# Kernel tuning notes

Measured on AMD Instinct MI355X. Metric: run time of the kernel, lower is better.

Reference implementation:

```python
import jax, jax.numpy as jnp
import numpy as np

D_MODEL = 64
D_K = 64
N_HEADS = 4
D_FF = 64
LN_EPS = 1e-5


def _layernorm(x, g, b):
    mu = jnp.mean(x, axis=-1, keepdims=True)
    var = jnp.var(x, axis=-1, keepdims=True)
    return (x - mu) * jax.lax.rsqrt(var + LN_EPS) * g + b


def setup_inputs() -> dict:
    key = jax.random.key(0)
    ks = jax.random.split(key, 20)
    B, L = 8, 2048
    s = 0.05
    inp = {
        "x": jax.random.normal(ks[0], (B, L, D_MODEL), jnp.float32),
        "attn_mask": jax.random.randint(ks[1], (B, L, L), 0, 2).astype(bool),
        "u": jax.random.normal(ks[2], (B, 1, D_MODEL), jnp.float32),
        "wq": jax.random.normal(ks[3], (D_MODEL, D_K * N_HEADS), jnp.float32) * s,
        "wk": jax.random.normal(ks[4], (D_MODEL, D_K * N_HEADS), jnp.float32) * s,
        "wv": jax.random.normal(ks[5], (D_MODEL, D_K * N_HEADS), jnp.float32) * s,
        "uqw": jax.random.normal(ks[6], (D_MODEL, D_K), jnp.float32) * s,
        "ukw": jax.random.normal(ks[7], (D_MODEL, D_K), jnp.float32) * s,
        "uvw": jax.random.normal(ks[8], (D_MODEL, D_K), jnp.float32) * s,
        "sq1": jax.random.normal(ks[9], (D_MODEL, D_MODEL // 2), jnp.float32) * s,
        "sq2": jax.random.normal(ks[10], (D_MODEL // 2, 1), jnp.float32) * s,
        "sk1": jax.random.normal(ks[11], (D_MODEL, D_MODEL // 2), jnp.float32) * s,
        "sk2": jax.random.normal(ks[12], (D_MODEL // 2, 1), jnp.float32) * s,
        "sv1": jax.random.normal(ks[13], (D_MODEL, D_MODEL // 2), jnp.float32) * s,
        "sv2": jax.random.normal(ks[14], (D_MODEL // 2, 1), jnp.float32) * s,
        "fcw": jax.random.normal(ks[15], (N_HEADS * D_K, D_MODEL), jnp.float32) * s,
        "ln1_g": jnp.ones((D_MODEL,), jnp.float32),
        "ln1_b": jnp.zeros((D_MODEL,), jnp.float32),
        "ffn1": jax.random.normal(ks[16], (D_MODEL, D_FF), jnp.float32) * s,
        "ffn2": jax.random.normal(ks[17], (D_FF, D_MODEL), jnp.float32) * s,
        "ln2_g": jnp.ones((D_MODEL,), jnp.float32),
        "ln2_b": jnp.zeros((D_MODEL,), jnp.float32),
    }
    return inp


def reference(x, attn_mask, u, wq, wk, wv, uqw, ukw, uvw, sq1, sq2, sk1, sk2,
              sv1, sv2, fcw, ln1_g, ln1_b, ffn1, ffn2, ln2_g, ln2_b):
    B, L, _ = x.shape
    H, dk = N_HEADS, D_K
    # per-head Q,K,V: [B,H,L,dk]
    Q = (x @ wq).reshape(B, L, H, dk).transpose(0, 2, 1, 3)
    K = (x @ wk).reshape(B, L, H, dk).transpose(0, 2, 1, 3)
    V = (x @ wv).reshape(B, L, H, dk).transpose(0, 2, 1, 3)
    # broadcast scalar gates from u: [B,1,1]
    S_q = jax.nn.relu(u @ sq1) @ sq2
    S_k = jax.nn.relu(u @ sk1) @ sk2
    S_v = jax.nn.relu(u @ sv1) @ sv2
    uQ = (x @ uqw) * S_q  # [B,L,dk]
    uK = (x @ ukw) * S_k
    uV = (x @ uvw) * S_v
    scores = (jnp.einsum('bhqd,bhkd->bhqk', Q, K)
              + jnp.einsum('bqd,bkd->bqk', uQ, uK)[:, None]) / jnp.sqrt(
                  jnp.asarray(dk, x.dtype))
    scores = jnp.where(attn_mask[:, None], jnp.asarray(-1e9, x.dtype), scores)
    attn = jax.nn.softmax(scores, axis=-1)  # [B,H,L,L]
    ctx = jnp.einsum('bhqk,bhkd->bhqd', attn, V + uV[:, None])
    ctx = ctx.transpose(0, 2, 1, 3).reshape(B, L, H * dk)
    out = ctx @ fcw  # dropout is identity in eval mode
    enc = _layernorm(out + x, ln1_g, ln1_b)
    ffn = jax.nn.relu(enc @ ffn1) @ ffn2
    res = _layernorm(ffn + enc, ln2_g, ln2_b)
    return (res, attn)
```

## Files before the change

kernel.cpp:

```cpp
#include <hip/hip_runtime.h>
#include <hip/hip_bf16.h>
#include <stdint.h>

typedef __bf16  bf16x8  __attribute__((ext_vector_type(8)));
typedef float   f32x4   __attribute__((ext_vector_type(4)));
typedef unsigned short u16x8 __attribute__((ext_vector_type(8)));
typedef unsigned short u16x4 __attribute__((ext_vector_type(4)));
typedef unsigned short ushort_t;

__device__ __forceinline__ unsigned short f2b(float f) {
    __hip_bfloat16 h = __float2bfloat16(f);
    return *reinterpret_cast<unsigned short*>(&h);
}

__device__ __forceinline__ void cp16(const void* g, void* l) {
    __builtin_amdgcn_global_load_lds(
        (const __attribute__((address_space(1))) unsigned int*)g,
        (__attribute__((address_space(3))) unsigned int*)l,
        16, 0, 0);
}

#define BB 8
#define LL 2048
#define DM 64
#define NH 4
#define DK 64

__global__ __launch_bounds__(256) void k_maskpack(const int* __restrict__ mask,
                                                  unsigned int* __restrict__ words) {
    int tid = blockIdx.x * 256 + threadIdx.x;
    const int4* p = reinterpret_cast<const int4*>(mask) + (size_t)tid * 8;
    unsigned int wbits = 0u;
    #pragma unroll
    for (int i = 0; i < 8; i++) {
        int4 v = p[i];
        wbits |= (v.x != 0 ? 1u << (4 * i + 0) : 0u);
        wbits |= (v.y != 0 ? 1u << (4 * i + 1) : 0u);
        wbits |= (v.z != 0 ? 1u << (4 * i + 2) : 0u);
        wbits |= (v.w != 0 ? 1u << (4 * i + 3) : 0u);
    }
    words[tid] = wbits;
}

__global__ __launch_bounds__(64) void k_gates(const float* __restrict__ u,
                                              const float* s1q, const float* s2q,
                                              const float* s1k, const float* s2k,
                                              const float* s1v, const float* s2v,
                                              float* __restrict__ gates) {
    int b = blockIdx.x, g = blockIdx.y, lane = threadIdx.x;
    const float* s1 = (g == 0) ? s1q : (g == 1) ? s1k : s1v;
    const float* s2 = (g == 0) ? s2q : (g == 1) ? s2k : s2v;
    float ur = u[b * 64 + lane];
    float acc = 0.f;
    for (int j = 0; j < 64; j++) {
        float uj = __shfl(ur, j, 64);
        if (lane < 32) acc += uj * s1[j * 32 + lane];
    }
    float r = (lane < 32) ? fmaxf(acc, 0.f) * s2[lane] : 0.f;
    for (int m = 32; m >= 1; m >>= 1) r += __shfl_xor(r, m, 64);
    if (lane == 0) gates[b * 3 + g] = r;
}

__global__ __launch_bounds__(256) void k_proj(const float* __restrict__ x,
                                              const float* __restrict__ wq,
                                              const float* __restrict__ wk,
                                              const float* __restrict__ wv,
                                              const float* __restrict__ uqw,
                                              const float* __restrict__ ukw,
                                              const float* __restrict__ uvw,
                                              const float* __restrict__ gates,
                                              ushort_t* __restrict__ Qe,
                                              ushort_t* __restrict__ Ke,
                                              ushort_t* __restrict__ VeT) {
    int lt = blockIdx.x, b = blockIdx.y, t = threadIdx.x;
    int l0 = lt * 32;
    __shared__ float lx[32][68];
    __shared__ float luv[32][68];
    #pragma unroll
    for (int i = 0; i < 2; i++) {
        int id = t + i * 256;
        int r = id >> 4, c4 = id & 15;
        float4 v = *(const float4*)&x[((b * LL) + l0 + r) * 64 + c4 * 4];
        *(float4*)&lx[r][c4 * 4] = v;
    }
    __syncthreads();
    float Sq = gates[b * 3 + 0], Sk = gates[b * 3 + 1], Sv = gates[b * 3 + 2];
    if (t < 192) {
        int m = t >> 6, d = t & 63;
        const float* uw = (m == 0) ? uqw : (m == 1) ? ukw : uvw;
        float acc[32];
        #pragma unroll
        for (int r = 0; r < 32; r++) acc[r] = 0.f;
        for (int j = 0; j < 64; j += 4) {
            float w0 = uw[(j + 0) * 64 + d], w1 = uw[(j + 1) * 64 + d];
            float w2 = uw[(j + 2) * 64 + d], w3 = uw[(j + 3) * 64 + d];
            #pragma unroll
            for (int r = 0; r < 32; r++) {
                float4 xv = *(const float4*)&lx[r][j];
                acc[r] += xv.x * w0 + xv.y * w1 + xv.z * w2 + xv.w * w3;
            }
        }
        if (m == 2) {
            #pragma unroll
            for (int r = 0; r < 32; r++) luv[r][d] = acc[r] * Sv;
        } else if (m == 0) {
            for (int r = 0; r < 32; r++) {
                unsigned short v = f2b(acc[r] * Sq * 0.125f);
                int base = ((b * NH) * LL + l0 + r) * 128 + 64 + d;
                #pragma unroll
                for (int hh2 = 0; hh2 < 4; hh2++) Qe[base + hh2 * (LL * 128)] = v;
            }
        } else {
            for (int r = 0; r < 32; r++) {
                unsigned short v = f2b(acc[r] * Sk);
                int col = 64 + (d ^ ((r & 7) << 3));
                int base = ((b * NH) * LL + l0 + r) * 128 + col;
                #pragma unroll
                for (int hh2 = 0; hh2 < 4; hh2++) Ke[base + hh2 * (LL * 128)] = v;
            }
        }
    }
    __syncthreads();
    int c = t, hh = c >> 6, d = c & 63;
    float aq_[32], ak_[32], av_[32];
    #pragma unroll
    for (int r = 0; r < 32; r++) { aq_[r] = 0.f; ak_[r] = 0.f; av_[r] = 0.f; }
    for (int j = 0; j < 64; j += 4) {
        float q0w = wq[(j + 0) * 256 + c], q1w = wq[(j + 1) * 256 + c];
        float q2w = wq[(j + 2) * 256 + c], q3w = wq[(j + 3) * 256 + c];
        float k0w = wk[(j + 0) * 256 + c], k1w = wk[(j + 1) * 256 + c];
        float k2w = wk[(j + 2) * 256 + c], k3w = wk[(j + 3) * 256 + c];
        float v0w = wv[(j + 0) * 256 + c], v1w = wv[(j + 1) * 256 + c];
        float v2w = wv[(j + 2) * 256 + c], v3w = wv[(j + 3) * 256 + c];
        #pragma unroll
        for (int r = 0; r < 32; r++) {
            float4 xv = *(const float4*)&lx[r][j];
            aq_[r] += xv.x * q0w + xv.y * q1w + xv.z * q2w + xv.w * q3w;
            ak_[r] += xv.x * k0w + xv.y * k1w + xv.z * k2w + xv.w * k3w;
            av_[r] += xv.x * v0w + xv.y * v1w + xv.z * v2w + xv.w * v3w;
        }
    }
    int outbase = (b * NH + hh) * LL + l0;
    #pragma unroll
    for (int r = 0; r < 32; r++) Qe[(outbase + r) * 128 + d] = f2b(aq_[r] * 0.125f);
    #pragma unroll
    for (int r = 0; r < 32; r++)
        Ke[(outbase + r) * 128 + (d ^ ((r & 7) << 3))] = f2b(ak_[r]);
    long vbase = ((long)(b * NH + hh) * 64 + d) * LL;
    int lblk = l0 & ~63, loff = l0 & 63;
    #pragma unroll
    for (int rb = 0; rb < 4; rb++) {
        u16x8 vv;
        #pragma unroll
        for (int k = 0; k < 8; k++) {
            int r = rb * 8 + k;
            vv[k] = f2b(av_[r] + luv[r][d]);
        }
        int off = (loff + rb * 8) ^ ((d & 7) << 3);
        *(u16x8*)&VeT[vbase + lblk + off] = vv;
    }
}

__global__ __launch_bounds__(256) void k_attn(const ushort_t* __restrict__ Qe,
                                              const ushort_t* __restrict__ Ke,
                                              const ushort_t* __restrict__ VeT,
                                              const unsigned int* __restrict__ mwords,
                                              float* __restrict__ ctx,
                                              float* __restrict__ attn) {
    int lin = blockIdx.x + 32 * blockIdx.y + 128 * blockIdx.z;
    int sw  = ((lin & 7) << 7) | (lin >> 3);
    int qt = sw & 31, h = (sw >> 5) & 3, b = sw >> 7;

    int t = threadIdx.x, w = t >> 6, lane = t & 63, quad = lane >> 4, l15 = lane & 15;
    int q0 = qt * 64;
    int bh = b * NH + h;
    const ushort_t* QeB = Qe + (long)bh * LL * 128;
    const ushort_t* KeB = Ke + (long)bh * LL * 128;
    const ushort_t* VtB = VeT + (long)bh * 64 * LL;
    float* attnB = attn + (long)bh * LL * LL;
    const unsigned int* mB = mwords + (long)(b * LL) * 64;

    __shared__ ushort_t sKe[2][64 * 128];
    __shared__ ushort_t sVT[2][64 * 64];
    __shared__ unsigned int smask[64][66];
    __shared__ ushort_t sPb[4][16][72];

    #pragma unroll
    for (int i = 0; i < 16; i++) {
        int id = t + i * 256;
        smask[id >> 6][id & 63] = mB[(q0 + (id >> 6)) * 64 + (id & 63)];
    }

    bf16x8 aq[4];
    int qrow = q0 + w * 16 + l15;
    #pragma unroll
    for (int c = 0; c < 4; c++)
        aq[c] = *(const bf16x8*)&QeB[qrow * 128 + c * 32 + quad * 8];

    int swz = (l15 & 7) << 3;
    float lsum = 0.f;

    #pragma unroll
    for (int i = 0; i < 4; i++) {
        int off = (t + i * 256) * 16;
        cp16((const char*)KeB + off, (char*)&sKe[0][0] + off);
    }
    for (int kt = 0; kt < 32; kt++) {
        int cur = kt & 1;
        __syncthreads();
        if (kt < 31) {
            size_t gb = (size_t)(kt + 1) * 64 * 256;
            #pragma unroll
            for (int i = 0; i < 4; i++) {
                int off = (t + i * 256) * 16;
                cp16((const char*)KeB + gb + off, (char*)&sKe[cur ^ 1][0] + off);
            }
        }
        #pragma unroll
        for (int nb = 0; nb < 4; nb++) {
            f32x4 s = (f32x4){0.f, 0.f, 0.f, 0.f};
            #pragma unroll
            for (int c = 0; c < 4; c++) {
                bf16x8 kb = *(const bf16x8*)&sKe[cur][(nb * 16 + l15) * 128 + ((c * 32 + quad * 8) ^ swz)];
                s = __builtin_amdgcn_mfma_f32_16x16x32_bf16(kb, aq[c], s, 0, 0, 0);
            }
            unsigned int word = smask[w * 16 + l15][kt * 2 + (nb >> 1)];
            #pragma unroll
            for (int reg = 0; reg < 4; reg++) {
                unsigned int bit = (word >> ((nb & 1) * 16 + quad * 4 + reg)) & 1u;
                lsum += bit ? 0.f : __expf(fminf(s[reg], 60.f));
            }
        }
    }
    {
        lsum += __shfl_xor(lsum, 16, 64);
        lsum += __shfl_xor(lsum, 32, 64);
    }
    float inv = (lsum > 0.f) ? 1.f / lsum : 0.f;
    float invC[4];
    #pragma unroll
    for (int reg = 0; reg < 4; reg++) invC[reg] = __shfl(inv, quad * 4 + reg, 16);

    f32x4 cacc[4];
    #pragma unroll
    for (int db = 0; db < 4; db++) cacc[db] = (f32x4){0.f, 0.f, 0.f, 0.f};

    #pragma unroll
    for (int i = 0; i < 4; i++) {
        int off = (t + i * 256) * 16;
        cp16((const char*)KeB + off, (char*)&sKe[0][0] + off);
    }
    #pragma unroll
    for (int i = 0; i < 2; i++) {
        int off = (t + i * 256) * 16;
        int d = off >> 7, cb = off & 127;
        cp16((const char*)VtB + (size_t)d * (LL * 2) + cb, (char*)&sVT[0][0] + off);
    }
    for (int kt = 0; kt < 32; kt++) {
        int cur = kt & 1;
        int k0 = kt * 64;
        __syncthreads();
        if (kt < 31) {
            size_t gKe = (size_t)(k0 + 64) * 256;
            #pragma unroll
            for (int i = 0; i < 4; i++) {
                int off = (t + i * 256) * 16;
                cp16((const char*)KeB + gKe + off, (char*)&sKe[cur ^ 1][0] + off);
            }
            #pragma unroll
            for (int i = 0; i < 2; i++) {
                int off = (t + i * 256) * 16;
                int d = off >> 7, cb = off & 127;
                cp16((const char*)VtB + (size_t)d * (LL * 2) + (size_t)(k0 + 64) * 2 + cb,
                     (char*)&sVT[cur ^ 1][0] + off);
            }
        }
        #pragma unroll
        for (int nb = 0; nb < 4; nb++) {
            f32x4 s = (f32x4){0.f, 0.f, 0.f, 0.f};
            #pragma unroll
            for (int c = 0; c < 4; c++) {
                bf16x8 kb = *(const bf16x8*)&sKe[cur][(nb * 16 + l15) * 128 + ((c * 32 + quad * 8) ^ swz)];
                s = __builtin_amdgcn_mfma_f32_16x16x32_bf16(kb, aq[c], s, 0, 0, 0);
            }
            unsigned int word = smask[w * 16 + l15][kt * 2 + (nb >> 1)];
            u16x4 pk;
            f32x4 st;
            #pragma unroll
            for (int reg = 0; reg < 4; reg++) {
                unsigned int bit = (word >> ((nb & 1) * 16 + quad * 4 + reg)) & 1u;
                float p = bit ? 0.f : __expf(fminf(s[reg], 60.f));
                pk[reg] = f2b(p);
                st[reg] = p * inv;
            }
            *(u16x4*)&sPb[w][l15][nb * 16 + quad * 4] = pk;
            __builtin_nontemporal_store(st,
                (f32x4*)&attnB[(long)(q0 + w * 16 + l15) * LL + k0 + nb * 16 + quad * 4]);
        }
        #pragma unroll
        for (int db = 0; db < 4; db++) {
            #pragma unroll
            for (int c2 = 0; c2 < 2; c2++) {
                bf16x8 a  = *(const bf16x8*)&sPb[w][l15][c2 * 32 + quad * 8];
                bf16x8 bb = *(const bf16x8*)&sVT[cur][(db * 16 + l15) * 64 + ((c2 * 32 + quad * 8) ^ swz)];
                cacc[db] = __builtin_amdgcn_mfma_f32_16x16x32_bf16(a, bb, cacc[db], 0, 0, 0);
            }
        }
    }
    #pragma unroll
    for (int db = 0; db < 4; db++)
        #pragma unroll
        for (int reg = 0; reg < 4; reg++) {
            int qr = q0 + w * 16 + quad * 4 + reg;
            ctx[((long)(b * LL) + qr) * 256 + h * 64 + db * 16 + l15] = cacc[db][reg] * invC[reg];
        }
}

__global__ __launch_bounds__(256) void k_epi(const float* __restrict__ ctx,
                                             const float* __restrict__ x,
                                             const float* __restrict__ fcw,
                                             const float* __restrict__ g1,
                                             const float* __restrict__ b1,
                                             const float* __restrict__ f1,
                                             const float* __restrict__ f2,
                                             const float* __restrict__ g2,
                                             const float* __restrict__ b2w,
                                             float* __restrict__ res) {
    int w = threadIdx.x >> 6, lane = threadIdx.x & 63;
    int row = blockIdx.x * 4 + w;
    const float* cr = ctx + (long)row * 256;
    float creg[4];
    #pragma unroll
    for (int i = 0; i < 4; i++) creg[i] = cr[i * 64 + lane];
    float acc = 0.f;
    #pragma unroll
    for (int j = 0; j < 256; j++) {
        float cj = __shfl(creg[j >> 6], j & 63, 64);
        acc += cj * fcw[j * 64 + lane];
    }
    float val = acc + x[row * 64 + lane];
    float mu = val;
    #pragma unroll
    for (int m = 1; m < 64; m <<= 1) mu += __shfl_xor(mu, m, 64);
    mu *= (1.f / 64.f);
    float d0 = val - mu;
    float var = d0 * d0;
    #pragma unroll
    for (int m = 1; m < 64; m <<= 1) var += __shfl_xor(var, m, 64);
    var *= (1.f / 64.f);
    float enc = d0 * rsqrtf(var + 1e-5f) * g1[lane] + b1[lane];
    float a1 = 0.f;
    #pragma unroll
    for (int j = 0; j < 64; j++) a1 += __shfl(enc, j, 64) * f1[j * 64 + lane];
    float hrel = fmaxf(a1, 0.f);
    float a2 = 0.f;
    #pragma unroll
    for (int j = 0; j < 64; j++) a2 += __shfl(hrel, j, 64) * f2[j * 64 + lane];
    float v2 = a2 + enc;
    float mu2 = v2;
    #pragma unroll
    for (int m = 1; m < 64; m <<= 1) mu2 += __shfl_xor(mu2, m, 64);
    mu2 *= (1.f / 64.f);
    float d2 = v2 - mu2;
    float var2 = d2 * d2;
    #pragma unroll
    for (int m = 1; m < 64; m <<= 1) var2 += __shfl_xor(var2, m, 64);
    var2 *= (1.f / 64.f);
    float outv = d2 * rsqrtf(var2 + 1e-5f) * g2[lane] + b2w[lane];
    res[row * 64 + lane] = outv;
}

extern "C" void kernel_launch(void* const* d_in, const int* in_sizes, int n_in,
                              void* d_out, int out_size, void* d_ws, size_t ws_size,
                              hipStream_t stream) {
    const float* x    = (const float*)d_in[0];
    const int*   mask = (const int*)d_in[1];
    const float* u    = (const float*)d_in[2];
    const float* wq   = (const float*)d_in[3];
    const float* wk   = (const float*)d_in[4];
    const float* wv   = (const float*)d_in[5];
    const float* uqw  = (const float*)d_in[6];
    const float* ukw  = (const float*)d_in[7];
    const float* uvw  = (const float*)d_in[8];
    const float* sq1  = (const float*)d_in[9];
    const float* sq2  = (const float*)d_in[10];
    const float* sk1  = (const float*)d_in[11];
    const float* sk2  = (const float*)d_in[12];
    const float* sv1  = (const float*)d_in[13];
    const float* sv2  = (const float*)d_in[14];
    const float* fcw  = (const float*)d_in[15];
    const float* g1   = (const float*)d_in[16];
    const float* b1   = (const float*)d_in[17];
    const float* f1   = (const float*)d_in[18];
    const float* f2   = (const float*)d_in[19];
    const float* g2   = (const float*)d_in[20];
    const float* b2w  = (const float*)d_in[21];

    char* ws = (char*)d_ws;
    float*        gates  = (float*)(ws + 0);
    unsigned int* mwords = (unsigned int*)(ws + 4096);
    ushort_t*     Qe     = (ushort_t*)(ws + 4198400);
    ushort_t*     Ke     = (ushort_t*)(ws + 20975616);
    ushort_t*     VeT    = (ushort_t*)(ws + 37752832);
    float*        ctx    = (float*)(ws + 46141440);

    float* res  = (float*)d_out;
    float* attn = (float*)d_out + (size_t)BB * LL * DM;

    k_maskpack<<<dim3(4096), dim3(256), 0, stream>>>(mask, mwords);
    k_gates<<<dim3(8, 3), dim3(64), 0, stream>>>(u, sq1, sq2, sk1, sk2, sv1, sv2, gates);
    k_proj<<<dim3(64, 8), dim3(256), 0, stream>>>(x, wq, wk, wv, uqw, ukw, uvw, gates, Qe, Ke, VeT);
    k_attn<<<dim3(32, 4, 8), dim3(256), 0, stream>>>(Qe, Ke, VeT, mwords, ctx, attn);
    k_epi<<<dim3(4096), dim3(256), 0, stream>>>(ctx, x, fcw, g1, b1, f1, f2, g2, b2w, res);
}
```

Measured before the change: 1.019 ms.

## Stream mask words via async LDS loads and coalesce attn stores through shared

Replaces the upfront load of the whole 64x64 mask-word tile into shared memory with a double-buffered async load of 4 words per row, issued every other key tile. The attention-probability stores are staged through a per-wave shared buffer so each global nontemporal store writes contiguous 128-byte row segments instead of scattered 16-byte pieces. This aims to improve coalescing of the dominant attn write stream and cut mask-loading overhead and LDS footprint. The cost is extra LDS traffic and possible bank conflicts on the staging buffer.

```diff
diff --git a/kernel.cpp b/kernel.cpp
--- a/kernel.cpp
+++ b/kernel.cpp
@@ -182,14 +182,9 @@
 
     __shared__ ushort_t sKe[2][64 * 128];
     __shared__ ushort_t sVT[2][64 * 64];
-    __shared__ unsigned int smask[64][66];
     __shared__ ushort_t sPb[4][16][72];
-
-    #pragma unroll
-    for (int i = 0; i < 16; i++) {
-        int id = t + i * 256;
-        smask[id >> 6][id & 63] = mB[(q0 + (id >> 6)) * 64 + (id & 63)];
-    }
+    __shared__ float    sSt[4][16][68];
+    __shared__ unsigned int msk[2][64][4];
 
     bf16x8 aq[4];
     int qrow = q0 + w * 16 + l15;
@@ -199,12 +194,15 @@
 
     int swz = (l15 & 7) << 3;
     float lsum = 0.f;
+    int srow = lane >> 3, scol = lane & 7;
 
     #pragma unroll
     for (int i = 0; i < 4; i++) {
         int off = (t + i * 256) * 16;
         cp16((const char*)KeB + off, (char*)&sKe[0][0] + off);
     }
+    if (w == 0)
+        cp16((const char*)&mB[(q0 + lane) * 64], (char*)&msk[0][0][0] + lane * 16);
     for (int kt = 0; kt < 32; kt++) {
         int cur = kt & 1;
         __syncthreads();
@@ -216,6 +214,10 @@
                 cp16((const char*)KeB + gb + off, (char*)&sKe[cur ^ 1][0] + off);
             }
         }
+        if ((kt & 1) == 0 && kt < 30 && w == 0)
+            cp16((const char*)&mB[(q0 + lane) * 64 + kt * 2 + 4],
+                 (char*)&msk[((kt >> 1) & 1) ^ 1][0][0] + lane * 16);
+        uint2 mw = *(const uint2*)&msk[(kt >> 1) & 1][w * 16 + l15][(kt & 1) * 2];
         #pragma unroll
         for (int nb = 0; nb < 4; nb++) {
             f32x4 s = (f32x4){0.f, 0.f, 0.f, 0.f};
@@ -224,7 +226,7 @@
                 bf16x8 kb = *(const bf16x8*)&sKe[cur][(nb * 16 + l15) * 128 + ((c * 32 + quad * 8) ^ swz)];
                 s = __builtin_amdgcn_mfma_f32_16x16x32_bf16(kb, aq[c], s, 0, 0, 0);
             }
-            unsigned int word = smask[w * 16 + l15][kt * 2 + (nb >> 1)];
+            unsigned int word = (nb & 2) ? mw.y : mw.x;
             #pragma unroll
             for (int reg = 0; reg < 4; reg++) {
                 unsigned int bit = (word >> ((nb & 1) * 16 + quad * 4 + reg)) & 1u;
@@ -256,6 +258,8 @@
         int d = off >> 7, cb = off & 127;
         cp16((const char*)VtB + (size_t)d * (LL * 2) + cb, (char*)&sVT[0][0] + off);
     }
+    if (w == 0)
+        cp16((const char*)&mB[(q0 + lane) * 64], (char*)&msk[0][0][0] + lane * 16);
     for (int kt = 0; kt < 32; kt++) {
         int cur = kt & 1;
         int k0 = kt * 64;
@@ -275,6 +279,10 @@
                      (char*)&sVT[cur ^ 1][0] + off);
             }
         }
+        if ((kt & 1) == 0 && kt < 30 && w == 0)
+            cp16((const char*)&mB[(q0 + lane) * 64 + kt * 2 + 4],
+                 (char*)&msk[((kt >> 1) & 1) ^ 1][0][0] + lane * 16);
+        uint2 mw = *(const uint2*)&msk[(kt >> 1) & 1][w * 16 + l15][(kt & 1) * 2];
         #pragma unroll
         for (int nb = 0; nb < 4; nb++) {
             f32x4 s = (f32x4){0.f, 0.f, 0.f, 0.f};
@@ -283,7 +291,7 @@
                 bf16x8 kb = *(const bf16x8*)&sKe[cur][(nb * 16 + l15) * 128 + ((c * 32 + quad * 8) ^ swz)];
                 s = __builtin_amdgcn_mfma_f32_16x16x32_bf16(kb, aq[c], s, 0, 0, 0);
             }
-            unsigned int word = smask[w * 16 + l15][kt * 2 + (nb >> 1)];
+            unsigned int word = (nb & 2) ? mw.y : mw.x;
             u16x4 pk;
             f32x4 st;
             #pragma unroll
@@ -294,9 +302,16 @@
                 st[reg] = p * inv;
             }
             *(u16x4*)&sPb[w][l15][nb * 16 + quad * 4] = pk;
-            __builtin_nontemporal_store(st,
-                (f32x4*)&attnB[(long)(q0 + w * 16 + l15) * LL + k0 + nb * 16 + quad * 4]);
-        }
+            *(f32x4*)&sSt[w][l15][nb * 16 + quad * 4] = st;
+        }
+        #pragma unroll
+        for (int jr = 0; jr < 2; jr++)
+            #pragma unroll
+            for (int jc = 0; jc < 2; jc++) {
+                f32x4 v = *(const f32x4*)&sSt[w][8 * jr + srow][jc * 32 + scol * 4];
+                __builtin_nontemporal_store(v,
+                    (f32x4*)&attnB[(long)(q0 + w * 16 + 8 * jr + srow) * LL + k0 + jc * 32 + scol * 4]);
+            }
         #pragma unroll
         for (int db = 0; db < 4; db++) {
             #pragma unroll
```

Measured after the change: 996.7 us. 1.02x faster.
